# Optimization experiments

Hardware: AMD Instinct MI355X
Metric: run time of the kernel (lower is better)

Reference implementation:

```python
import jax, jax.numpy as jnp
import numpy as np

N_NODES = 100000
N_EDGES = 1600000
IN_F = 128
OUT_F = 32


def setup_inputs() -> dict:
    key = jax.random.key(0)
    k1, k2, k3 = jax.random.split(key, 3)
    x = jax.random.normal(k1, (N_NODES, IN_F), dtype=jnp.float32)
    edge_index = jax.random.randint(k2, (2, N_EDGES), 0, N_NODES, dtype=jnp.int64)
    W = jax.random.normal(k3, (OUT_F, IN_F), dtype=jnp.float32) * 0.1
    b = jnp.zeros((OUT_F,), dtype=jnp.float32)
    return {"x": x, "edge_index": edge_index, "W": W, "b": b}


def reference(x, edge_index, W, b):
    # PyG GCNConv: add self-loops, symmetric normalization, linear, aggregate, bias
    N = x.shape[0]
    loops = jnp.arange(N, dtype=edge_index.dtype)
    src = jnp.concatenate([edge_index[0], loops])  # message source j
    dst = jnp.concatenate([edge_index[1], loops])  # aggregation target i
    ones = jnp.ones(src.shape[0], dtype=x.dtype)
    deg = jax.ops.segment_sum(ones, dst, num_segments=N)  # deg computed at col (target)
    dis = jnp.where(deg > 0, jax.lax.rsqrt(deg), 0.0)  # deg^{-1/2}, inf -> 0
    norm = dis[src] * dis[dst]  # [E+N]
    h = x @ W.T  # [N, OUT_F] linear transform first (PyG order)
    msg = h[src] * norm[:, None]  # [E+N, OUT_F] gathered, normalized messages
    out = jax.ops.segment_sum(msg, dst, num_segments=N)  # scatter-add aggregate
    return out + b
```

## Files before the change

### kernel.cpp

```cpp
#include <hip/hip_runtime.h>

#define IN_F 128
#define OUT_F 32
#define BKT_SHIFT 9
#define BKT_NODES 512
#define NBKT 196
#define PART_CHUNK 4096
#define SORT_CAP 12288
#define GEMM_NPB 128

typedef unsigned int uint32;
typedef __attribute__((ext_vector_type(8))) short bf16x8;
typedef __attribute__((ext_vector_type(4))) float f32x4;

__device__ __forceinline__ float bf2f(uint32 u) {
    union { uint32 ui; float f; } c; c.ui = u << 16; return c.f;
}
__device__ __forceinline__ uint32 f2bf(float x) {
    union { float f; uint32 ui; } c; c.f = x;
    uint32 u = c.ui;
    u += 0x7fffu + ((u >> 16) & 1u);
    return u >> 16;
}
__device__ __forceinline__ bf16x8 pack8(float4 lo, float4 hi) {
    union { bf16x8 v; uint32 u[4]; } r;
    r.u[0] = f2bf(lo.x) | (f2bf(lo.y) << 16);
    r.u[1] = f2bf(lo.z) | (f2bf(lo.w) << 16);
    r.u[2] = f2bf(hi.x) | (f2bf(hi.y) << 16);
    r.u[3] = f2bf(hi.z) | (f2bf(hi.w) << 16);
    return r.v;
}

__global__ void __launch_bounds__(512) k_phist(const int* __restrict__ dst,
        int* __restrict__ T, int E, int EB) {
    __shared__ int h[256];
    int t = threadIdx.x;
    if (t < 256) h[t] = 0;
    __syncthreads();
    int base = blockIdx.x * PART_CHUNK;
    #pragma unroll
    for (int i = 0; i < 8; ++i) {
        int e = base + i * 512 + t;
        if (e < E) atomicAdd(&h[dst[e] >> BKT_SHIFT], 1);
    }
    __syncthreads();
    if (t < NBKT) T[t * EB + blockIdx.x] = h[t];
}

__global__ void __launch_bounds__(256) k_oscan_a(
        int* __restrict__ T, int* __restrict__ partials, int M) {
    __shared__ int sc[256];
    int t = threadIdx.x;
    int base = blockIdx.x * 512;
    int i0 = base + 2 * t, i1 = i0 + 1;
    int d0 = (i0 < M) ? T[i0] : 0;
    int d1 = (i1 < M) ? T[i1] : 0;
    sc[t] = d0 + d1;
    __syncthreads();
    #pragma unroll
    for (int ofs = 1; ofs < 256; ofs <<= 1) {
        int v = sc[t];
        int u = (t >= ofs) ? sc[t - ofs] : 0;
        __syncthreads();
        sc[t] = v + u;
        __syncthreads();
    }
    int eT = t ? sc[t - 1] : 0;
    if (i0 < M) T[i0] = eT;
    if (i1 < M) T[i1] = eT + d0;
    if (t == 0) partials[blockIdx.x] = sc[255];
}

__global__ void __launch_bounds__(256) k_oscan_b(
        const int* __restrict__ partials, int* __restrict__ bases, int nb) {
    __shared__ int sc[256];
    int t = threadIdx.x;
    sc[t] = (t < nb) ? partials[t] : 0;
    __syncthreads();
    #pragma unroll
    for (int ofs = 1; ofs < 256; ofs <<= 1) {
        int v = sc[t];
        int u = (t >= ofs) ? sc[t - ofs] : 0;
        __syncthreads();
        sc[t] = v + u;
        __syncthreads();
    }
    bases[t] = t ? sc[t - 1] : 0;
}

__global__ void __launch_bounds__(512) k_part(
        const int* __restrict__ src, const int* __restrict__ dst,
        const int* __restrict__ T, const int* __restrict__ obases,
        uint32* __restrict__ pk, int E, int EB) {
    __shared__ int    hist[256];
    __shared__ int    sc[256];
    __shared__ int    cbase[256];
    __shared__ int    gbase[256];
    __shared__ uint32 stage[PART_CHUNK];
    int t = threadIdx.x;
    if (t < 256) hist[t] = 0;
    __syncthreads();
    int base = blockIdx.x * PART_CHUNK;

    int bkt[8], rank[8];
    uint32 val[8];
    #pragma unroll
    for (int i = 0; i < 8; ++i) {
        int e = base + i * 512 + t;
        if (e < E) {
            int d = dst[e];
            int s = src[e];
            int b = d >> BKT_SHIFT;
            bkt[i] = b;
            val[i] = (uint32)s | ((uint32)(d & (BKT_NODES - 1)) << 17);
            rank[i] = atomicAdd(&hist[b], 1);
        } else {
            bkt[i] = -1;
        }
    }
    __syncthreads();
    if (t < 256) sc[t] = hist[t];
    __syncthreads();
    #pragma unroll
    for (int ofs = 1; ofs < 256; ofs <<= 1) {
        int v = 0, u = 0;
        if (t < 256) { v = sc[t]; u = (t >= ofs) ? sc[t - ofs] : 0; }
        __syncthreads();
        if (t < 256) sc[t] = v + u;
        __syncthreads();
    }
    if (t < 256) cbase[t] = t ? sc[t - 1] : 0;
    if (t < NBKT) {
        int idx = t * EB + blockIdx.x;
        gbase[t] = T[idx] + obases[idx >> 9];
    }
    __syncthreads();
    #pragma unroll
    for (int i = 0; i < 8; ++i)
        if (bkt[i] >= 0) stage[cbase[bkt[i]] + rank[i]] = val[i];
    __syncthreads();
    int wave = t >> 6, lane = t & 63;
    for (int b = wave; b < NBKT; b += 8) {
        int cnt_b = hist[b];
        int cb = cbase[b], gb = gbase[b];
        for (int s = lane; s < cnt_b; s += 64)
            pk[gb + s] = stage[cb + s];
    }
}

__global__ void __launch_bounds__(512) k_sg(
        uint32* __restrict__ pk, const int* __restrict__ T,
        const int* __restrict__ obases, int* __restrict__ cursor,
        float* __restrict__ dis,
        const float* __restrict__ x, const float* __restrict__ W,
        unsigned short* __restrict__ gbf, int n, int E, int EB) {
    if (blockIdx.x < NBKT) {
        __shared__ uint32 stg[SORT_CAP];
        __shared__ int    cnt[BKT_NODES];
        __shared__ int    sc[256];
        int b = blockIdx.x, t = threadIdx.x;
        int nodeBase = b * BKT_NODES;
        int i0 = b * EB;
        int start = T[i0] + obases[i0 >> 9];
        int end;
        if (b + 1 < NBKT) {
            int i1 = (b + 1) * EB;
            end = T[i1] + obases[i1 >> 9];
        } else {
            end = E;
        }
        int len = end - start;
        if (t < BKT_NODES) cnt[t] = 0;
        __syncthreads();
        for (int i = t; i < len; i += 512) atomicAdd(&cnt[pk[start + i] >> 17], 1);
        __syncthreads();
        int c0 = 0, c1 = 0;
        if (t < 256) { c0 = cnt[2 * t]; c1 = cnt[2 * t + 1]; sc[t] = c0 + c1; }
        __syncthreads();
        #pragma unroll
        for (int ofs = 1; ofs < 256; ofs <<= 1) {
            int v = 0, u = 0;
            if (t < 256) { v = sc[t]; u = (t >= ofs) ? sc[t - ofs] : 0; }
            __syncthreads();
            if (t < 256) sc[t] = v + u;
            __syncthreads();
        }
        if (t < 256) {
            int eT = t ? sc[t - 1] : 0;
            cnt[2 * t]     = eT;
            cnt[2 * t + 1] = eT + c0;
            int n0 = nodeBase + 2 * t;
            if (n0 < n) {
                cursor[n0] = start + eT;
                dis[n0] = rsqrtf((float)(c0 + 1));
                int n1 = n0 + 1;
                if (n1 < n) {
                    cursor[n1] = start + eT + c0;
                    dis[n1] = rsqrtf((float)(c1 + 1));
                }
            }
        }
        __syncthreads();
        for (int i = t; i < len; i += 512) {
            uint32 p = pk[start + i];
            int pos = atomicAdd(&cnt[p >> 17], 1);
            stg[pos] = p & 0x1FFFFu;
        }
        __syncthreads();
        for (int i = t; i < len; i += 512) pk[start + i] = stg[i];
    } else {
        int gid = blockIdx.x - NBKT;
        int lane = threadIdx.x & 63;
        int wv   = threadIdx.x >> 6;
        int nodeBase = gid * GEMM_NPB + wv * 16;
        int r16 = lane & 15;
        int kg  = lane >> 4;
        int arow = nodeBase + r16;
        if (arow >= n) arow = n - 1;
        const float4* xr = (const float4*)(x + (size_t)arow * IN_F);
        bf16x8 afr[4];
        #pragma unroll
        for (int kk = 0; kk < 4; ++kk) {
            int c4 = kk * 8 + kg * 2;
            afr[kk] = pack8(xr[c4], xr[c4 + 1]);
        }
        bf16x8 bfr[2][4];
        #pragma unroll
        for (int fb = 0; fb < 2; ++fb) {
            const float4* wr = (const float4*)(W + (size_t)(fb * 16 + r16) * IN_F);
            #pragma unroll
            for (int kk = 0; kk < 4; ++kk) {
                int c4 = kk * 8 + kg * 2;
                bfr[fb][kk] = pack8(wr[c4], wr[c4 + 1]);
            }
        }
        f32x4 acc0 = {0.f, 0.f, 0.f, 0.f};
        f32x4 acc1 = {0.f, 0.f, 0.f, 0.f};
        #pragma unroll
        for (int kk = 0; kk < 4; ++kk) {
            acc0 = __builtin_amdgcn_mfma_f32_16x16x32_bf16(afr[kk], bfr[0][kk], acc0, 0, 0, 0);
            acc1 = __builtin_amdgcn_mfma_f32_16x16x32_bf16(afr[kk], bfr[1][kk], acc1, 0, 0, 0);
        }
        #pragma unroll
        for (int j = 0; j < 4; ++j) {
            int node = nodeBase + kg * 4 + j;
            if (node < n) {
                gbf[node * OUT_F + r16]      = (unsigned short)f2bf(acc0[j]);
                gbf[node * OUT_F + 16 + r16] = (unsigned short)f2bf(acc1[j]);
            }
        }
    }
}

__global__ void __launch_bounds__(256) k_aggr(
        const uint32* __restrict__ g2, const uint32* __restrict__ pk,
        const int* __restrict__ cursor, const float* __restrict__ dis,
        const float* __restrict__ b, float* __restrict__ out, int n, int E) {
    int tid = threadIdx.x;
    int node = blockIdx.x * 16 + (tid >> 4);
    if (node >= n) return;
    int l = tid & 15;
    int start = cursor[node];
    int end   = (node + 1 < n) ? cursor[node + 1] : E;
    float dd = dis[node];
    uint32 vs = g2[node * 16 + l];
    float ax = bf2f(vs & 0xffffu) * dd;
    float ay = bf2f(vs >> 16) * dd;
    float bx = 0.f, by = 0.f;
    int e = start;
    for (; e + 4 <= end; e += 4) {
        int s0 = pk[e], s1 = pk[e + 1], s2 = pk[e + 2], s3 = pk[e + 3];
        uint32 v0 = g2[s0 * 16 + l];
        uint32 v1 = g2[s1 * 16 + l];
        uint32 v2 = g2[s2 * 16 + l];
        uint32 v3 = g2[s3 * 16 + l];
        float w0 = dis[s0], w1 = dis[s1], w2 = dis[s2], w3 = dis[s3];
        ax += bf2f(v0 & 0xffffu) * w0; ay += bf2f(v0 >> 16) * w0;
        bx += bf2f(v1 & 0xffffu) * w1; by += bf2f(v1 >> 16) * w1;
        ax += bf2f(v2 & 0xffffu) * w2; ay += bf2f(v2 >> 16) * w2;
        bx += bf2f(v3 & 0xffffu) * w3; by += bf2f(v3 >> 16) * w3;
    }
    for (; e < end; ++e) {
        int s = pk[e];
        uint32 v = g2[s * 16 + l];
        float w = dis[s];
        ax += bf2f(v & 0xffffu) * w; ay += bf2f(v >> 16) * w;
    }
    float2 bb = ((const float2*)b)[l];
    float2 o;
    o.x = dd * (ax + bx) + bb.x;
    o.y = dd * (ay + by) + bb.y;
    ((float2*)out)[node * 16 + l] = o;
}

extern "C" void kernel_launch(void* const* d_in, const int* in_sizes, int n_in,
                              void* d_out, int out_size, void* d_ws, size_t ws_size,
                              hipStream_t stream) {
    const float* x  = (const float*)d_in[0];
    const int*   ei = (const int*)d_in[1];
    const float* W  = (const float*)d_in[2];
    const float* b  = (const float*)d_in[3];
    float* out = (float*)d_out;

    int N = in_sizes[0] / IN_F;
    int E = in_sizes[1] / 2;
    const int* src = ei;
    const int* dst = ei + E;

    int EB = (E + PART_CHUNK - 1) / PART_CHUNK;
    int M  = NBKT * EB;

    char* p = (char*)d_ws;
    int*            T        = (int*)p;            p += ((size_t)M * 4 + 255) & ~255ull;
    int*            partials = (int*)p;            p += 2048;
    int*            obases   = (int*)p;            p += 2048;
    int*            cursor   = (int*)p;            p += ((size_t)N * 4 + 255) & ~255ull;
    float*          dis      = (float*)p;          p += ((size_t)N * 4 + 255) & ~255ull;
    uint32*         pkbuf    = (uint32*)p;         p += ((size_t)E * 4 + 255) & ~255ull;
    unsigned short* gbf      = (unsigned short*)p; p += ((size_t)N * OUT_F * 2 + 255) & ~255ull;

    int nsb = (M + 511) / 512;
    int gemmBlocks = (N + GEMM_NPB - 1) / GEMM_NPB;

    k_phist<<<EB, 512, 0, stream>>>(dst, T, E, EB);
    k_oscan_a<<<nsb, 256, 0, stream>>>(T, partials, M);
    k_oscan_b<<<1, 256, 0, stream>>>(partials, obases, nsb);
    k_part<<<EB, 512, 0, stream>>>(src, dst, T, obases, pkbuf, E, EB);
    k_sg<<<NBKT + gemmBlocks, 512, 0, stream>>>(
        pkbuf, T, obases, cursor, dis, x, W, gbf, N, E, EB);
    k_aggr<<<(N + 15) / 16, 256, 0, stream>>>(
        (const uint32*)gbf, pkbuf, cursor, dis, b, out, N, E);
}
```

Before: 162.2 us.

## Use per-wave LDS histograms in partitioning and 8-byte gathers in aggregation

The histogram and partition kernels now give each wave its own LDS histogram. This cuts contention on shared atomics, and the per-wave counts are prefix-combined so the staging offsets stay exact. The aggregation kernel now uses 8 lanes per node, each loading 4 bf16 features as a uint2, so each block handles twice as many nodes with wider loads. The costs are more LDS per block, an extra per-wave scan step, and fewer lanes per node issuing gathers.

```diff
diff --git a/kernel.cpp b/kernel.cpp
--- a/kernel.cpp
+++ b/kernel.cpp
@@ -33,18 +33,24 @@
 
 __global__ void __launch_bounds__(512) k_phist(const int* __restrict__ dst,
         int* __restrict__ T, int E, int EB) {
-    __shared__ int h[256];
+    __shared__ int h8[8][256];
     int t = threadIdx.x;
-    if (t < 256) h[t] = 0;
+    int wv = t >> 6;
+    for (int i = t; i < 8 * 256; i += 512) ((int*)h8)[i] = 0;
     __syncthreads();
     int base = blockIdx.x * PART_CHUNK;
     #pragma unroll
     for (int i = 0; i < 8; ++i) {
         int e = base + i * 512 + t;
-        if (e < E) atomicAdd(&h[dst[e] >> BKT_SHIFT], 1);
-    }
-    __syncthreads();
-    if (t < NBKT) T[t * EB + blockIdx.x] = h[t];
+        if (e < E) atomicAdd(&h8[wv][dst[e] >> BKT_SHIFT], 1);
+    }
+    __syncthreads();
+    if (t < NBKT) {
+        int s = 0;
+        #pragma unroll
+        for (int w = 0; w < 8; ++w) s += h8[w][t];
+        T[t * EB + blockIdx.x] = s;
+    }
 }
 
 __global__ void __launch_bounds__(256) k_oscan_a(
@@ -92,13 +98,15 @@
         const int* __restrict__ src, const int* __restrict__ dst,
         const int* __restrict__ T, const int* __restrict__ obases,
         uint32* __restrict__ pk, int E, int EB) {
-    __shared__ int    hist[256];
+    __shared__ int    h8[8][256];
+    __shared__ int    hTot[256];
     __shared__ int    sc[256];
     __shared__ int    cbase[256];
     __shared__ int    gbase[256];
     __shared__ uint32 stage[PART_CHUNK];
     int t = threadIdx.x;
-    if (t < 256) hist[t] = 0;
+    int wv = t >> 6;
+    for (int i = t; i < 8 * 256; i += 512) ((int*)h8)[i] = 0;
     __syncthreads();
     int base = blockIdx.x * PART_CHUNK;
 
@@ -113,13 +121,23 @@
             int b = d >> BKT_SHIFT;
             bkt[i] = b;
             val[i] = (uint32)s | ((uint32)(d & (BKT_NODES - 1)) << 17);
-            rank[i] = atomicAdd(&hist[b], 1);
+            rank[i] = atomicAdd(&h8[wv][b], 1);
         } else {
             bkt[i] = -1;
         }
     }
     __syncthreads();
-    if (t < 256) sc[t] = hist[t];
+    if (t < 256) {
+        int run = 0;
+        #pragma unroll
+        for (int w = 0; w < 8; ++w) {
+            int tmp = h8[w][t];
+            h8[w][t] = run;
+            run += tmp;
+        }
+        hTot[t] = run;
+        sc[t] = run;
+    }
     __syncthreads();
     #pragma unroll
     for (int ofs = 1; ofs < 256; ofs <<= 1) {
@@ -137,11 +155,11 @@
     __syncthreads();
     #pragma unroll
     for (int i = 0; i < 8; ++i)
-        if (bkt[i] >= 0) stage[cbase[bkt[i]] + rank[i]] = val[i];
+        if (bkt[i] >= 0) stage[cbase[bkt[i]] + h8[wv][bkt[i]] + rank[i]] = val[i];
     __syncthreads();
     int wave = t >> 6, lane = t & 63;
     for (int b = wave; b < NBKT; b += 8) {
-        int cnt_b = hist[b];
+        int cnt_b = hTot[b];
         int cb = cbase[b], gb = gbase[b];
         for (int s = lane; s < cnt_b; s += 64)
             pk[gb + s] = stage[cb + s];
@@ -257,40 +275,50 @@
         const int* __restrict__ cursor, const float* __restrict__ dis,
         const float* __restrict__ b, float* __restrict__ out, int n, int E) {
     int tid = threadIdx.x;
-    int node = blockIdx.x * 16 + (tid >> 4);
+    int node = blockIdx.x * 32 + (tid >> 3);
     if (node >= n) return;
-    int l = tid & 15;
+    int l = tid & 7;
+    const uint2* g2v = (const uint2*)g2;
     int start = cursor[node];
     int end   = (node + 1 < n) ? cursor[node + 1] : E;
     float dd = dis[node];
-    uint32 vs = g2[node * 16 + l];
-    float ax = bf2f(vs & 0xffffu) * dd;
-    float ay = bf2f(vs >> 16) * dd;
-    float bx = 0.f, by = 0.f;
+    uint2 vs = g2v[node * 8 + l];
+    float a0 = bf2f(vs.x & 0xffffu) * dd;
+    float a1 = bf2f(vs.x >> 16) * dd;
+    float a2 = bf2f(vs.y & 0xffffu) * dd;
+    float a3 = bf2f(vs.y >> 16) * dd;
+    float c0 = 0.f, c1 = 0.f, c2 = 0.f, c3 = 0.f;
     int e = start;
     for (; e + 4 <= end; e += 4) {
         int s0 = pk[e], s1 = pk[e + 1], s2 = pk[e + 2], s3 = pk[e + 3];
-        uint32 v0 = g2[s0 * 16 + l];
-        uint32 v1 = g2[s1 * 16 + l];
-        uint32 v2 = g2[s2 * 16 + l];
-        uint32 v3 = g2[s3 * 16 + l];
+        uint2 v0 = g2v[s0 * 8 + l];
+        uint2 v1 = g2v[s1 * 8 + l];
+        uint2 v2 = g2v[s2 * 8 + l];
+        uint2 v3 = g2v[s3 * 8 + l];
         float w0 = dis[s0], w1 = dis[s1], w2 = dis[s2], w3 = dis[s3];
-        ax += bf2f(v0 & 0xffffu) * w0; ay += bf2f(v0 >> 16) * w0;
-        bx += bf2f(v1 & 0xffffu) * w1; by += bf2f(v1 >> 16) * w1;
-        ax += bf2f(v2 & 0xffffu) * w2; ay += bf2f(v2 >> 16) * w2;
-        bx += bf2f(v3 & 0xffffu) * w3; by += bf2f(v3 >> 16) * w3;
+        a0 += bf2f(v0.x & 0xffffu) * w0; a1 += bf2f(v0.x >> 16) * w0;
+        a2 += bf2f(v0.y & 0xffffu) * w0; a3 += bf2f(v0.y >> 16) * w0;
+        c0 += bf2f(v1.x & 0xffffu) * w1; c1 += bf2f(v1.x >> 16) * w1;
+        c2 += bf2f(v1.y & 0xffffu) * w1; c3 += bf2f(v1.y >> 16) * w1;
+        a0 += bf2f(v2.x & 0xffffu) * w2; a1 += bf2f(v2.x >> 16) * w2;
+        a2 += bf2f(v2.y & 0xffffu) * w2; a3 += bf2f(v2.y >> 16) * w2;
+        c0 += bf2f(v3.x & 0xffffu) * w3; c1 += bf2f(v3.x >> 16) * w3;
+        c2 += bf2f(v3.y & 0xffffu) * w3; c3 += bf2f(v3.y >> 16) * w3;
     }
     for (; e < end; ++e) {
         int s = pk[e];
-        uint32 v = g2[s * 16 + l];
+        uint2 v = g2v[s * 8 + l];
         float w = dis[s];
-        ax += bf2f(v & 0xffffu) * w; ay += bf2f(v >> 16) * w;
-    }
-    float2 bb = ((const float2*)b)[l];
-    float2 o;
-    o.x = dd * (ax + bx) + bb.x;
-    o.y = dd * (ay + by) + bb.y;
-    ((float2*)out)[node * 16 + l] = o;
+        a0 += bf2f(v.x & 0xffffu) * w; a1 += bf2f(v.x >> 16) * w;
+        a2 += bf2f(v.y & 0xffffu) * w; a3 += bf2f(v.y >> 16) * w;
+    }
+    float4 bb = ((const float4*)b)[l];
+    float4 o;
+    o.x = dd * (a0 + c0) + bb.x;
+    o.y = dd * (a1 + c1) + bb.y;
+    o.z = dd * (a2 + c2) + bb.z;
+    o.w = dd * (a3 + c3) + bb.w;
+    ((float4*)out)[node * 8 + l] = o;
 }
 
 extern "C" void kernel_launch(void* const* d_in, const int* in_sizes, int n_in,
@@ -328,6 +356,6 @@
     k_part<<<EB, 512, 0, stream>>>(src, dst, T, obases, pkbuf, E, EB);
     k_sg<<<NBKT + gemmBlocks, 512, 0, stream>>>(
         pkbuf, T, obases, cursor, dis, x, W, gbf, N, E, EB);
-    k_aggr<<<(N + 15) / 16, 256, 0, stream>>>(
+    k_aggr<<<(N + 31) / 32, 256, 0, stream>>>(
         (const uint32*)gbf, pkbuf, cursor, dis, b, out, N, E);
 }
```

After: 159.6 us. Within noise of the previous version (-1.6%).
